# Kernel optimization log

Hardware: AMD Instinct MI355X
Metric: run time of the kernel (lower is better)

## Reference

```python
import jax, jax.numpy as jnp
from jax import lax
import numpy as np

N = 4096      # nnodes
D = 64        # embed_dim
R = 128       # nodes per region
G = N // R    # 32 regions (contiguous blocks)
BIG = 1e9     # 'no edge' cost (scipy MST treats zero-similarity entries as absent edges)


def setup_inputs() -> dict:
    key = jax.random.key(0)
    emb = jax.random.normal(key, (N, D), dtype=jnp.float32) * 0.05  # nn.Embedding weight (xavier-like scale)
    region_id = jnp.arange(N) // R
    inter_mask = (region_id[:, None] != region_id[None, :]).astype(jnp.float32)  # block off-diagonal buffer
    return {"emb_weight": emb, "inter_mask": inter_mask, "inter_budget": 1024}


def _prim_forest_mask(W):
    """Prim's algorithm on dense cost matrix W [R,R] (BIG = missing edge).
    Returns symmetric 0/1 minimum-spanning-FOREST edge mask, matching
    scipy.sparse.csgraph.minimum_spanning_tree on the same graph (weights distinct)."""
    r = W.shape[0]

    def step(carry, _):
        in_tree, key_, parent, mask = carry
        km = jnp.where(in_tree, BIG, key_)
        u = jnp.argmin(km)                          # cheapest node to attach
        valid = (km[u] < BIG * 0.5).astype(W.dtype)  # BIG key => start new component, no edge
        p = parent[u]
        mask = mask.at[u, p].add(valid)
        mask = mask.at[p, u].add(valid)
        in_tree = in_tree.at[u].set(True)
        wu = W[u]
        improve = (~in_tree) & (wu < key_)
        key_ = jnp.where(improve, wu, key_)
        parent = jnp.where(improve, u, parent)
        return (in_tree, key_, parent, mask), None

    in_tree0 = jnp.zeros(r, dtype=bool).at[0].set(True)
    key0 = W[0]
    parent0 = jnp.zeros(r, dtype=jnp.int32)
    mask0 = jnp.zeros_like(W)
    (_, _, _, mask), _ = lax.scan(step, (in_tree0, key0, parent0, mask0), None, length=r - 1)
    return (mask > 0).astype(W.dtype)


def reference(emb_weight, inter_mask, inter_budget):
    # adj_dense = relu(tanh(E E^T))  [N,N]
    adj = jax.nn.relu(jnp.tanh(emb_weight @ emb_weight.T))
    adj_ng = lax.stop_gradient(adj)  # torch: MST input is .detach(); top-k indices carry no grad

    # ---- intra: per-region MST (max spanning forest of similarity == min SF of -sim) ----
    blocks = adj_ng.reshape(G, R, G, R)[jnp.arange(G), :, jnp.arange(G), :]  # [G,R,R] diagonal blocks
    eye = jnp.eye(R, dtype=bool)
    W = jnp.where((blocks > 0) & ~eye, -blocks, BIG)  # zero similarity => no edge (scipy semantics)
    intra_blocks = jax.vmap(_prim_forest_mask)(W)     # [G,R,R]
    idx = jnp.arange(N).reshape(G, R)
    intra = jnp.zeros((N, N), adj.dtype).at[idx[:, :, None], idx[:, None, :]].set(intra_blocks)
    intra = intra * (1.0 - jnp.eye(N, dtype=adj.dtype))  # fill_diagonal_(0)

    # ---- inter: global top-k over upper-triangular masked similarities ----
    flat = jnp.triu(adj_ng * inter_mask, k=1).reshape(-1)  # [N*N]
    k = int(inter_budget)  # == min(budget, nnz(inter_mask)//2); budget is smaller by construction
    _, top_idx = lax.top_k(flat, k)
    inter_sel = jnp.zeros(N * N, adj.dtype).at[top_idx].set(1.0).reshape(N, N)
    inter_sel = inter_sel + inter_sel.T

    final_mask = ((intra + inter_sel) > 0).astype(adj.dtype)
    return adj * final_mask
```

## Files before the change

kernel.cpp:

```cpp
#include <hip/hip_runtime.h>

#define NN 4096
#define DD 64
#define RR 128
#define GG 32
constexpr float BIGF = 1e9f;
constexpr unsigned BIGH = 0xCE6E6B28u;
constexpr unsigned FLOOR_KEY = 0x3D000000u;
constexpr int FLOORB = 0x3D0;
constexpr int NBINS  = 64;

constexpr int WS_FH   = 0;
constexpr int WS_ECNT = 2051;
constexpr int WS_CCNT = 2052;
constexpr int WS_MIJ  = 2112;
constexpr int WS_MV   = WS_MIJ + 4096;
constexpr int WS_EI   = WS_MV + 4096;
constexpr int WS_EJ   = WS_EI + 8192;
constexpr int WS_EV   = WS_EJ + 8192;
constexpr int WS_CK   = WS_EV + 8192;
constexpr int WS_CI   = WS_CK + 8192;
constexpr int EDGE_CAP = 8192;
constexpr int CAND_CAP = 8192;

__global__ void init_kernel(unsigned* ws) {
  for (int b = threadIdx.x; b < 2112; b += 1024) ws[b] = 0;
}

__device__ __forceinline__ void pair_decode(int p, int& gi, int& gj) {
  gi = 0;
  int rem = p;
  while (rem >= GG - 1 - gi) { rem -= GG - 1 - gi; ++gi; }
  gj = gi + 1 + rem;
}

__device__ __forceinline__ void scan_bins(const unsigned* __restrict__ ws, unsigned k,
                                          unsigned* shm ,
                                          unsigned& tlo, unsigned& thi, unsigned& rem) {
  const int t = threadIdx.x;
  if (t < NBINS) shm[t] = ws[WS_FH + FLOORB + t];
  __syncthreads();
  if (t == 0) {
    unsigned cum = 0;
    int fb = FLOORB;
    unsigned r = 0;
    for (int b = NBINS - 1; b >= 0; --b) {
      unsigned c = shm[b];
      if (cum + c >= k) { fb = FLOORB + b; r = k - cum; break; }
      cum += c;
    }
    shm[64] = ((unsigned)fb) << 20;
    shm[65] = ((unsigned)(fb + 1)) << 20;
    shm[66] = r;
  }
  __syncthreads();
  tlo = shm[64];
  thi = shm[65];
  rem = shm[66];
}

__global__ __launch_bounds__(256) void gemm_adj_kernel(const float* __restrict__ E,
                                                       float* __restrict__ adj,
                                                       unsigned* __restrict__ ws) {
  const int ti = blockIdx.y, tj = blockIdx.x;
  const bool rdiag = (ti >> 1) == (tj >> 1);
  if (tj < ti && !rdiag) return;
  const bool cross = (tj >> 1) > (ti >> 1);

  __shared__ float4 As4[64 * 16];
  __shared__ float4 Bs4[64 * 16];
  __shared__ unsigned h[NBINS];
  const float4* E4 = (const float4*)E;
  const int bi = ti * 64, bj = tj * 64;
  const int tid = threadIdx.x;

  if (tid < NBINS) h[tid] = 0;

#pragma unroll
  for (int it = 0; it < 4; ++it) {
    int row = (tid >> 4) + it * 16;
    int g = tid & 15;
    int sw = g ^ ((row >> 2) & 7);
    As4[row * 16 + sw] = E4[(bi + row) * 16 + g];
    Bs4[row * 16 + sw] = E4[(bj + row) * 16 + g];
  }
  __syncthreads();

  const int i0 = (tid >> 4) * 4;
  const int j0 = (tid & 15) * 4;
  const int sa = (i0 >> 2) & 7;
  const int sb = (j0 >> 2) & 7;
  float acc[4][4] = {};
#pragma unroll 2
  for (int k4 = 0; k4 < 16; ++k4) {
    float4 av[4], bv[4];
#pragma unroll
    for (int r = 0; r < 4; ++r) av[r] = As4[(i0 + r) * 16 + (k4 ^ sa)];
#pragma unroll
    for (int c = 0; c < 4; ++c) bv[c] = Bs4[(j0 + c) * 16 + (k4 ^ sb)];
#pragma unroll
    for (int r = 0; r < 4; ++r)
#pragma unroll
      for (int c = 0; c < 4; ++c) {
        acc[r][c] += av[r].x * bv[c].x;
        acc[r][c] += av[r].y * bv[c].y;
        acc[r][c] += av[r].z * bv[c].z;
        acc[r][c] += av[r].w * bv[c].w;
      }
  }
#pragma unroll
  for (int r = 0; r < 4; ++r) {
    float4 o;
    float* p = &o.x;
#pragma unroll
    for (int c = 0; c < 4; ++c) {
      float t = tanhf(acc[r][c]);
      p[c] = t > 0.f ? t : 0.f;
    }
    *(float4*)(adj + (size_t)(bi + i0 + r) * NN + bj + j0) = o;
    if (cross) {
#pragma unroll
      for (int c = 0; c < 4; ++c) {
        unsigned key = __float_as_uint(p[c]);
        if (key >= FLOOR_KEY) atomicAdd(&h[(key >> 20) - FLOORB], 1u);
      }
    }
  }
  if (cross) {
    __syncthreads();
    if (tid < NBINS) {
      unsigned c = h[tid];
      if (c) atomicAdd(&ws[WS_FH + FLOORB + tid], c);
    }
  }
}

template <int CTRL>
__device__ __forceinline__ unsigned dpp_umin(unsigned v) {
  unsigned o = (unsigned)__builtin_amdgcn_update_dpp((int)v, (int)v, CTRL, 0xF, 0xF, false);
  return o < v ? o : v;
}
__device__ __forceinline__ unsigned xfneg(float a) {
  return ~__float_as_uint(a) & 0x7FFFFFFFu;
}

__global__ __launch_bounds__(64) void mst_kernel(const float* __restrict__ adj, unsigned* ws) {
  __shared__ float W[RR * RR];
  __shared__ unsigned emij[RR];
  __shared__ float emv[RR];
  const int g = blockIdx.x, l = threadIdx.x, base = g * RR;
  float4* W4 = (float4*)W;
  const float4* A4 = (const float4*)adj;

#pragma unroll
  for (int n = 0; n < 64; ++n) {
    int f = l + 64 * n;
    W4[f] = A4[(size_t)(base + (f >> 5)) * (NN / 4) + (base >> 2) + (f & 31)];
  }
  emij[l] = 0xFFFFFFFFu;
  emij[l + 64] = 0xFFFFFFFFu;
  __syncthreads();

  const int n0 = l, n1 = l + 64;
  float a0 = W[n0], a1 = W[n1];
  unsigned key0 = (n0 != 0 && a0 > 0.f) ? xfneg(a0) : BIGH;
  unsigned key1 = (a1 > 0.f) ? xfneg(a1) : BIGH;
  bool in0 = (l == 0), in1 = false;
  int par0 = 0, par1 = 0;

  for (int it = 0; it < RR - 1; ++it) {
    const unsigned kA = in0 ? BIGH : key0;
    const unsigned kB = in1 ? BIGH : key1;
    unsigned km = kA < kB ? kA : kB;
    km = dpp_umin<0xB1>(km);
    km = dpp_umin<0x4E>(km);
    km = dpp_umin<0x141>(km);
    km = dpp_umin<0x140>(km);
    km = dpp_umin<0x142>(km);
    km = dpp_umin<0x143>(km);
    const unsigned m = (unsigned)__builtin_amdgcn_readlane((int)km, 63);

    const unsigned long long b0 = __ballot(kA == m);
    const unsigned long long b1 = __ballot(kB == m);
    const int u = b0 ? (__ffsll((unsigned long long)b0) - 1)
                     : (64 + __ffsll((unsigned long long)b1) - 1);

    const int p0 = __builtin_amdgcn_readlane(par0, u & 63);
    const int p1 = __builtin_amdgcn_readlane(par1, u & 63);
    const int par = (u >> 6) ? p1 : p0;
    if (l == 0) {
      unsigned pij = 0xFFFFFFFFu;
      float pv = 0.f;
      if ((int)m >= 0) {
        pij = ((unsigned)(base + u) << 12) | (unsigned)(base + par);
        pv = __uint_as_float(~m & 0x7FFFFFFFu);
      }
      emij[it] = pij;
      emv[it] = pv;
    }
    in0 = in0 || (u == n0);
    in1 = in1 || (u == n1);
    float w0v = W[u * RR + n0];
    float w1v = W[u * RR + n1];
    unsigned w0 = (w0v > 0.f && n0 != u) ? xfneg(w0v) : BIGH;
    unsigned w1 = (w1v > 0.f && n1 != u) ? xfneg(w1v) : BIGH;
    if (!in0 && w0 < key0) { key0 = w0; par0 = u; }
    if (!in1 && w1 < key1) { key1 = w1; par1 = u; }
  }
  __syncthreads();
  ws[WS_MIJ + base + l] = emij[l];
  ws[WS_MIJ + base + 64 + l] = emij[64 + l];
  ((float*)(ws + WS_MV))[base + l] = emv[l];
  ((float*)(ws + WS_MV))[base + 64 + l] = emv[64 + l];
}

__global__ __launch_bounds__(256) void collect_kernel(const float* __restrict__ adj,
                                                      unsigned* ws, const int* budget) {
  __shared__ unsigned shm[67];
  unsigned tlo, thi, rem;
  scan_bins(ws, (unsigned)budget[0], shm, tlo, thi, rem);
  (void)rem;
  int gi, gj;
  pair_decode(blockIdx.x, gi, gj);
  const float4* a4 = (const float4*)adj;
  for (int e = threadIdx.x; e < RR * 32; e += 256) {
    int r = e >> 5, c4 = e & 31;
    float4 v = a4[(size_t)(gi * RR + r) * (NN / 4) + gj * 32 + c4];
    float comp[4] = {v.x, v.y, v.z, v.w};
#pragma unroll
    for (int c = 0; c < 4; ++c) {
      float x = comp[c];
      if (!(x > 0.f)) continue;
      unsigned key = __float_as_uint(x);
      if (key < tlo) continue;
      int i = gi * RR + r, j = gj * RR + c4 * 4 + c;
      if (key >= thi) {
        unsigned slot = atomicAdd(ws + WS_ECNT, 1u);
        if (slot < EDGE_CAP) {
          ((int*)(ws + WS_EI))[slot] = i;
          ((int*)(ws + WS_EJ))[slot] = j;
          ((float*)(ws + WS_EV))[slot] = x;
        }
      } else {
        unsigned s2 = atomicAdd(ws + WS_CCNT, 1u);
        if (s2 < CAND_CAP) {
          ws[WS_CK + s2] = key;
          ws[WS_CI + s2] = (unsigned)((i << 12) | j);
        }
      }
    }
  }
}

__global__ __launch_bounds__(1024) void topk_kernel(unsigned* ws, const int* budget) {
  __shared__ unsigned long long s[CAND_CAP];
  __shared__ unsigned shm[67];
  unsigned tlo, thi, rem;
  scan_bins(ws, (unsigned)budget[0], shm, tlo, thi, rem);
  (void)tlo; (void)thi;
  const int t = threadIdx.x;
  unsigned n = ws[WS_CCNT];
  if (n > CAND_CAP) n = CAND_CAP;
  unsigned m = 2;
  while (m < n) m <<= 1;
  for (int i = t; i < (int)m; i += 1024) {
    unsigned long long v = 0ull;
    if (i < (int)n)
      v = ((unsigned long long)ws[WS_CK + i] << 32) |
          (unsigned long long)(0x00FFFFFFu - ws[WS_CI + i]);
    s[i] = v;
  }
  for (unsigned size = 2; size <= m; size <<= 1)
    for (unsigned stride = size >> 1; stride; stride >>= 1) {
      __syncthreads();
      for (unsigned i = t; i < m / 2; i += 1024) {
        unsigned lo = ((i & ~(stride - 1)) << 1) | (i & (stride - 1));
        unsigned hi = lo | stride;
        bool up = ((lo & size) == 0);
        unsigned long long a = s[lo], b = s[hi];
        if ((a > b) == up) { s[lo] = b; s[hi] = a; }
      }
    }
  __syncthreads();
  for (unsigned p = t; p < rem; p += 1024) {
    unsigned long long v = s[m - 1 - p];
    if (v == 0ull) continue;
    unsigned key = (unsigned)(v >> 32);
    unsigned idx = 0x00FFFFFFu - (unsigned)(v & 0xFFFFFFFFull);
    unsigned slot = atomicAdd(ws + WS_ECNT, 1u);
    if (slot < EDGE_CAP) {
      ((int*)(ws + WS_EI))[slot] = (int)(idx >> 12);
      ((int*)(ws + WS_EJ))[slot] = (int)(idx & 4095u);
      ((float*)(ws + WS_EV))[slot] = __uint_as_float(key);
    }
  }
}

__global__ __launch_bounds__(256) void zero_scatter_kernel(const unsigned* __restrict__ ws,
                                                           float* __restrict__ out) {
  const int bid = blockIdx.x;
  const int r0 = bid * 16;
  float4* out4 = (float4*)(out + (size_t)r0 * NN);
  const float4 z = make_float4(0.f, 0.f, 0.f, 0.f);
  for (int e = threadIdx.x; e < 16 * (NN / 4); e += 256) out4[e] = z;
  __syncthreads();
  unsigned cnt = ws[WS_ECNT];
  if (cnt > EDGE_CAP) cnt = EDGE_CAP;
  const int tot = 4096 + (int)cnt;
  for (int e = threadIdx.x; e < tot; e += 256) {
    int i, j;
    float v;
    if (e < 4096) {
      unsigned pij = ws[WS_MIJ + e];
      if (pij == 0xFFFFFFFFu) continue;
      i = (int)(pij >> 12);
      j = (int)(pij & 4095u);
      v = ((const float*)(ws + WS_MV))[e];
    } else {
      int q = e - 4096;
      i = ((const int*)(ws + WS_EI))[q];
      j = ((const int*)(ws + WS_EJ))[q];
      v = ((const float*)(ws + WS_EV))[q];
    }
    if ((i >> 4) == bid) out[(size_t)i * NN + j] = v;
    if ((j >> 4) == bid) out[(size_t)j * NN + i] = v;
  }
}

extern "C" void kernel_launch(void* const* d_in, const int* in_sizes, int n_in,
                              void* d_out, int out_size, void* d_ws, size_t ws_size,
                              hipStream_t stream) {
  const float* E      = (const float*)d_in[0];
  const int*   budget = (const int*)d_in[2];
  float*    adj = (float*)d_out;
  unsigned* ws  = (unsigned*)d_ws;

  init_kernel<<<1, 1024, 0, stream>>>(ws);
  gemm_adj_kernel<<<dim3(NN / 64, NN / 64), 256, 0, stream>>>(E, adj, ws);
  mst_kernel<<<GG, 64, 0, stream>>>(adj, ws);
  collect_kernel<<<GG * (GG - 1) / 2, 256, 0, stream>>>(adj, ws, budget);
  topk_kernel<<<1, 1024, 0, stream>>>(ws, budget);
  zero_scatter_kernel<<<256, 256, 0, stream>>>(ws, adj);
}
```

Before: 252.9 us.

## Compact top-k candidates inside GEMM epilogue and drop collect pass over adj

The GEMM epilogue for cross-region tiles no longer stores tanh values to adj. Instead it compacts entries above the histogram floor into a global candidate buffer, using a wave-level DPP prefix sum and one atomic per wave. A new filter kernel then scans only that buffer rather than rereading the upper triangle of adj, which is meant to cut global memory traffic on both the write and read side. The MST loop also gains two small changes: a readlane-based final reduction replaces the row broadcasts, and emitted edges are kept in registers instead of LDS. The cost is a candidate buffer of up to 16 MB, and correctness depends on the downstream scatter never needing the skipped adj values.

Measured after the change: 308.8 us. 22.1% more time.

```diff
diff --git a/kernel.cpp b/kernel.cpp
--- a/kernel.cpp
+++ b/kernel.cpp
@@ -4,34 +4,29 @@
 #define DD 64
 #define RR 128
 #define GG 32
-constexpr float BIGF = 1e9f;
 constexpr unsigned BIGH = 0xCE6E6B28u;
 constexpr unsigned FLOOR_KEY = 0x3D000000u;
 constexpr int FLOORB = 0x3D0;
 constexpr int NBINS  = 64;
 
-constexpr int WS_FH   = 0;
-constexpr int WS_ECNT = 2051;
-constexpr int WS_CCNT = 2052;
-constexpr int WS_MIJ  = 2112;
-constexpr int WS_MV   = WS_MIJ + 4096;
-constexpr int WS_EI   = WS_MV + 4096;
-constexpr int WS_EJ   = WS_EI + 8192;
-constexpr int WS_EV   = WS_EJ + 8192;
-constexpr int WS_CK   = WS_EV + 8192;
-constexpr int WS_CI   = WS_CK + 8192;
+constexpr int WS_FH      = 0;
+constexpr int WS_ECNT    = 2051;
+constexpr int WS_TCNT    = 2052;
+constexpr int WS_CANDCNT = 2053;
+constexpr int WS_MIJ     = 2112;
+constexpr int WS_MV      = WS_MIJ + 4096;
+constexpr int WS_EI      = WS_MV + 4096;
+constexpr int WS_EJ      = WS_EI + 8192;
+constexpr int WS_EV      = WS_EJ + 8192;
+constexpr int WS_CK      = WS_EV + 8192;
+constexpr int WS_CI      = WS_CK + 8192;
+constexpr int WS_CAND    = 65536;
 constexpr int EDGE_CAP = 8192;
 constexpr int CAND_CAP = 8192;
+constexpr unsigned CANDBUF_CAP = 2u * 1024u * 1024u;
 
 __global__ void init_kernel(unsigned* ws) {
   for (int b = threadIdx.x; b < 2112; b += 1024) ws[b] = 0;
-}
-
-__device__ __forceinline__ void pair_decode(int p, int& gi, int& gj) {
-  gi = 0;
-  int rem = p;
-  while (rem >= GG - 1 - gi) { rem -= GG - 1 - gi; ++gi; }
-  gj = gi + 1 + rem;
 }
 
 __device__ __forceinline__ void scan_bins(const unsigned* __restrict__ ws, unsigned k,
@@ -59,6 +54,19 @@
   rem = shm[66];
 }
 
+template <int CTRL>
+__device__ __forceinline__ unsigned dpp_umin(unsigned v) {
+  unsigned o = (unsigned)__builtin_amdgcn_update_dpp((int)v, (int)v, CTRL, 0xF, 0xF, false);
+  return o < v ? o : v;
+}
+template <int CTRL, int RMASK>
+__device__ __forceinline__ unsigned dpp_scanadd(unsigned v) {
+  return v + (unsigned)__builtin_amdgcn_update_dpp(0, (int)v, CTRL, RMASK, 0xF, false);
+}
+__device__ __forceinline__ unsigned xfneg(float a) {
+  return ~__float_as_uint(a) & 0x7FFFFFFFu;
+}
+
 __global__ __launch_bounds__(256) void gemm_adj_kernel(const float* __restrict__ E,
                                                        float* __restrict__ adj,
                                                        unsigned* __restrict__ ws) {
@@ -109,24 +117,57 @@
       }
   }
 #pragma unroll
-  for (int r = 0; r < 4; ++r) {
-    float4 o;
-    float* p = &o.x;
+  for (int r = 0; r < 4; ++r)
 #pragma unroll
     for (int c = 0; c < 4; ++c) {
       float t = tanhf(acc[r][c]);
-      p[c] = t > 0.f ? t : 0.f;
-    }
-    *(float4*)(adj + (size_t)(bi + i0 + r) * NN + bj + j0) = o;
-    if (cross) {
+      acc[r][c] = t > 0.f ? t : 0.f;
+    }
+
+  if (!cross) {
+#pragma unroll
+    for (int r = 0; r < 4; ++r) {
+      float4 o = make_float4(acc[r][0], acc[r][1], acc[r][2], acc[r][3]);
+      *(float4*)(adj + (size_t)(bi + i0 + r) * NN + bj + j0) = o;
+    }
+  } else {
+    const int lane = tid & 63;
+    unsigned cnt = 0;
+#pragma unroll
+    for (int r = 0; r < 4; ++r)
 #pragma unroll
       for (int c = 0; c < 4; ++c) {
-        unsigned key = __float_as_uint(p[c]);
-        if (key >= FLOOR_KEY) atomicAdd(&h[(key >> 20) - FLOORB], 1u);
-      }
-    }
-  }
-  if (cross) {
+        unsigned key = __float_as_uint(acc[r][c]);
+        if (key >= FLOOR_KEY) {
+          atomicAdd(&h[(key >> 20) - FLOORB], 1u);
+          ++cnt;
+        }
+      }
+    unsigned incl = cnt;
+    incl = dpp_scanadd<0x111, 0xF>(incl);
+    incl = dpp_scanadd<0x112, 0xF>(incl);
+    incl = dpp_scanadd<0x114, 0xF>(incl);
+    incl = dpp_scanadd<0x118, 0xF>(incl);
+    incl = dpp_scanadd<0x142, 0xA>(incl);
+    incl = dpp_scanadd<0x143, 0xC>(incl);
+    const unsigned tot = (unsigned)__builtin_amdgcn_readlane((int)incl, 63);
+    unsigned gbase = 0;
+    if (lane == 63 && tot) gbase = atomicAdd(ws + WS_CANDCNT, tot);
+    gbase = (unsigned)__builtin_amdgcn_readlane((int)gbase, 63);
+    unsigned off = gbase + (incl - cnt);
+    unsigned long long* cb = (unsigned long long*)(ws + WS_CAND);
+#pragma unroll
+    for (int r = 0; r < 4; ++r)
+#pragma unroll
+      for (int c = 0; c < 4; ++c) {
+        unsigned key = __float_as_uint(acc[r][c]);
+        if (key >= FLOOR_KEY) {
+          unsigned ij = (unsigned)(((bi + i0 + r) << 12) | (bj + j0 + c));
+          if (off < CANDBUF_CAP)
+            cb[off] = ((unsigned long long)key << 32) | ij;
+          ++off;
+        }
+      }
     __syncthreads();
     if (tid < NBINS) {
       unsigned c = h[tid];
@@ -135,19 +176,8 @@
   }
 }
 
-template <int CTRL>
-__device__ __forceinline__ unsigned dpp_umin(unsigned v) {
-  unsigned o = (unsigned)__builtin_amdgcn_update_dpp((int)v, (int)v, CTRL, 0xF, 0xF, false);
-  return o < v ? o : v;
-}
-__device__ __forceinline__ unsigned xfneg(float a) {
-  return ~__float_as_uint(a) & 0x7FFFFFFFu;
-}
-
 __global__ __launch_bounds__(64) void mst_kernel(const float* __restrict__ adj, unsigned* ws) {
   __shared__ float W[RR * RR];
-  __shared__ unsigned emij[RR];
-  __shared__ float emv[RR];
   const int g = blockIdx.x, l = threadIdx.x, base = g * RR;
   float4* W4 = (float4*)W;
   const float4* A4 = (const float4*)adj;
@@ -157,8 +187,6 @@
     int f = l + 64 * n;
     W4[f] = A4[(size_t)(base + (f >> 5)) * (NN / 4) + (base >> 2) + (f & 31)];
   }
-  emij[l] = 0xFFFFFFFFu;
-  emij[l + 64] = 0xFFFFFFFFu;
   __syncthreads();
 
   const int n0 = l, n1 = l + 64;
@@ -167,6 +195,8 @@
   unsigned key1 = (a1 > 0.f) ? xfneg(a1) : BIGH;
   bool in0 = (l == 0), in1 = false;
   int par0 = 0, par1 = 0;
+  unsigned e0ij = 0xFFFFFFFFu, e1ij = 0xFFFFFFFFu;
+  float e0v = 0.f, e1v = 0.f;
 
   for (int it = 0; it < RR - 1; ++it) {
     const unsigned kA = in0 ? BIGH : key0;
@@ -176,9 +206,13 @@
     km = dpp_umin<0x4E>(km);
     km = dpp_umin<0x141>(km);
     km = dpp_umin<0x140>(km);
-    km = dpp_umin<0x142>(km);
-    km = dpp_umin<0x143>(km);
-    const unsigned m = (unsigned)__builtin_amdgcn_readlane((int)km, 63);
+    const unsigned r0 = (unsigned)__builtin_amdgcn_readlane((int)km, 15);
+    const unsigned r1 = (unsigned)__builtin_amdgcn_readlane((int)km, 31);
+    const unsigned r2 = (unsigned)__builtin_amdgcn_readlane((int)km, 47);
+    const unsigned r3 = (unsigned)__builtin_amdgcn_readlane((int)km, 63);
+    const unsigned ma = r0 < r1 ? r0 : r1;
+    const unsigned mb = r2 < r3 ? r2 : r3;
+    const unsigned m = ma < mb ? ma : mb;
 
     const unsigned long long b0 = __ballot(kA == m);
     const unsigned long long b1 = __ballot(kB == m);
@@ -188,16 +222,16 @@
     const int p0 = __builtin_amdgcn_readlane(par0, u & 63);
     const int p1 = __builtin_amdgcn_readlane(par1, u & 63);
     const int par = (u >> 6) ? p1 : p0;
-    if (l == 0) {
-      unsigned pij = 0xFFFFFFFFu;
-      float pv = 0.f;
-      if ((int)m >= 0) {
-        pij = ((unsigned)(base + u) << 12) | (unsigned)(base + par);
-        pv = __uint_as_float(~m & 0x7FFFFFFFu);
-      }
-      emij[it] = pij;
-      emv[it] = pv;
-    }
+    unsigned pij = 0xFFFFFFFFu;
+    float pv = 0.f;
+    if ((int)m >= 0) {
+      pij = ((unsigned)(base + u) << 12) | (unsigned)(base + par);
+      pv = __uint_as_float(~m & 0x7FFFFFFFu);
+    }
+    const bool mine = (l == (it & 63));
+    if (it & 64) { if (mine) { e1ij = pij; e1v = pv; } }
+    else         { if (mine) { e0ij = pij; e0v = pv; } }
+
     in0 = in0 || (u == n0);
     in1 = in1 || (u == n1);
     float w0v = W[u * RR + n0];
@@ -207,46 +241,38 @@
     if (!in0 && w0 < key0) { key0 = w0; par0 = u; }
     if (!in1 && w1 < key1) { key1 = w1; par1 = u; }
   }
-  __syncthreads();
-  ws[WS_MIJ + base + l] = emij[l];
-  ws[WS_MIJ + base + 64 + l] = emij[64 + l];
-  ((float*)(ws + WS_MV))[base + l] = emv[l];
-  ((float*)(ws + WS_MV))[base + 64 + l] = emv[64 + l];
-}
-
-__global__ __launch_bounds__(256) void collect_kernel(const float* __restrict__ adj,
-                                                      unsigned* ws, const int* budget) {
+  ws[WS_MIJ + base + l] = e0ij;
+  ws[WS_MIJ + base + 64 + l] = e1ij;
+  ((float*)(ws + WS_MV))[base + l] = e0v;
+  ((float*)(ws + WS_MV))[base + 64 + l] = e1v;
+}
+
+__global__ __launch_bounds__(256) void filt_kernel(unsigned* ws, const int* budget) {
   __shared__ unsigned shm[67];
   unsigned tlo, thi, rem;
   scan_bins(ws, (unsigned)budget[0], shm, tlo, thi, rem);
   (void)rem;
-  int gi, gj;
-  pair_decode(blockIdx.x, gi, gj);
-  const float4* a4 = (const float4*)adj;
-  for (int e = threadIdx.x; e < RR * 32; e += 256) {
-    int r = e >> 5, c4 = e & 31;
-    float4 v = a4[(size_t)(gi * RR + r) * (NN / 4) + gj * 32 + c4];
-    float comp[4] = {v.x, v.y, v.z, v.w};
-#pragma unroll
-    for (int c = 0; c < 4; ++c) {
-      float x = comp[c];
-      if (!(x > 0.f)) continue;
-      unsigned key = __float_as_uint(x);
-      if (key < tlo) continue;
-      int i = gi * RR + r, j = gj * RR + c4 * 4 + c;
-      if (key >= thi) {
-        unsigned slot = atomicAdd(ws + WS_ECNT, 1u);
-        if (slot < EDGE_CAP) {
-          ((int*)(ws + WS_EI))[slot] = i;
-          ((int*)(ws + WS_EJ))[slot] = j;
-          ((float*)(ws + WS_EV))[slot] = x;
-        }
-      } else {
-        unsigned s2 = atomicAdd(ws + WS_CCNT, 1u);
-        if (s2 < CAND_CAP) {
-          ws[WS_CK + s2] = key;
-          ws[WS_CI + s2] = (unsigned)((i << 12) | j);
-        }
+  unsigned cnt = ws[WS_CANDCNT];
+  if (cnt > CANDBUF_CAP) cnt = CANDBUF_CAP;
+  const unsigned long long* cb = (const unsigned long long*)(ws + WS_CAND);
+  const unsigned stride = gridDim.x * blockDim.x;
+  for (unsigned idx = blockIdx.x * blockDim.x + threadIdx.x; idx < cnt; idx += stride) {
+    unsigned long long v = cb[idx];
+    unsigned key = (unsigned)(v >> 32);
+    if (key < tlo) continue;
+    unsigned ij = (unsigned)v;
+    if (key >= thi) {
+      unsigned slot = atomicAdd(ws + WS_ECNT, 1u);
+      if (slot < EDGE_CAP) {
+        ((int*)(ws + WS_EI))[slot] = (int)(ij >> 12);
+        ((int*)(ws + WS_EJ))[slot] = (int)(ij & 4095u);
+        ((float*)(ws + WS_EV))[slot] = __uint_as_float(key);
+      }
+    } else {
+      unsigned s2 = atomicAdd(ws + WS_TCNT, 1u);
+      if (s2 < CAND_CAP) {
+        ws[WS_CK + s2] = key;
+        ws[WS_CI + s2] = ij;
       }
     }
   }
@@ -259,7 +285,7 @@
   scan_bins(ws, (unsigned)budget[0], shm, tlo, thi, rem);
   (void)tlo; (void)thi;
   const int t = threadIdx.x;
-  unsigned n = ws[WS_CCNT];
+  unsigned n = ws[WS_TCNT];
   if (n > CAND_CAP) n = CAND_CAP;
   unsigned m = 2;
   while (m < n) m <<= 1;
@@ -338,7 +364,7 @@
   init_kernel<<<1, 1024, 0, stream>>>(ws);
   gemm_adj_kernel<<<dim3(NN / 64, NN / 64), 256, 0, stream>>>(E, adj, ws);
   mst_kernel<<<GG, 64, 0, stream>>>(adj, ws);
-  collect_kernel<<<GG * (GG - 1) / 2, 256, 0, stream>>>(adj, ws, budget);
+  filt_kernel<<<1024, 256, 0, stream>>>(ws, budget);
   topk_kernel<<<1, 1024, 0, stream>>>(ws, budget);
   zero_scatter_kernel<<<256, 256, 0, stream>>>(ws, adj);
 }
```
